# Kernel tuning notes

Measured on AMD Instinct MI355X. Metric: run time of the kernel, lower is better.

## Reference

```python
import jax, jax.numpy as jnp
import numpy as np

B, S, D = 4, 2048, 2048
H = 16
DH = D // H  # 128


def setup_inputs() -> dict:
    key = jax.random.key(0)
    ks = jax.random.split(key, 12)
    s = 1.0 / np.sqrt(D)
    inp = {
        "Q": jax.random.normal(ks[0], (B, S, D), jnp.float32),
        "K": jax.random.normal(ks[1], (B, S, D), jnp.float32),
        "V": jax.random.normal(ks[2], (B, S, D), jnp.float32),
        "mask": jnp.tril(jnp.ones((S, S), jnp.int32))[None, None],  # causal [1,1,S,S]
        "wq": jax.random.uniform(ks[3], (D, D), jnp.float32, -s, s),
        "bq": jax.random.uniform(ks[4], (D,), jnp.float32, -s, s),
        "wk": jax.random.uniform(ks[5], (D, D), jnp.float32, -s, s),
        "bk": jax.random.uniform(ks[6], (D,), jnp.float32, -s, s),
        "wv": jax.random.uniform(ks[7], (D, D), jnp.float32, -s, s),
        "bv": jax.random.uniform(ks[8], (D,), jnp.float32, -s, s),
        "wo": jax.random.uniform(ks[9], (D, D), jnp.float32, -s, s),
        "bo": jax.random.uniform(ks[10], (D,), jnp.float32, -s, s),
    }
    return inp


def _split_heads(x):
    # [B,S,D] -> [B,H,S,DH]
    b, s, _ = x.shape
    return x.reshape(b, s, H, DH).transpose(0, 2, 1, 3)


def reference(Q, K, V, mask, wq, bq, wk, bk, wv, bv, wo, bo):
    q = _split_heads(Q @ wq + bq)
    k = _split_heads(K @ wk + bk)
    v = _split_heads(V @ wv + bv)
    scores = jnp.einsum("bhqd,bhkd->bhqk", q, k) / jnp.sqrt(jnp.float32(DH))
    scores = jnp.where(mask == 0, jnp.float32(-1e9), scores)
    probs = jax.nn.softmax(scores, axis=-1)
    attn = jnp.einsum("bhqk,bhkd->bhqd", probs, v)  # [B,H,S,DH]
    attn = attn.transpose(0, 2, 1, 3).reshape(Q.shape[0], Q.shape[1], D)
    return attn @ wo + bo
```

## Files before the change

kernel.cpp:

```cpp
#include <hip/hip_runtime.h>
#include <hip/hip_bf16.h>

typedef __attribute__((ext_vector_type(8))) short short8;
typedef __attribute__((ext_vector_type(4))) float f32x4;

#define DEVINL __device__ __forceinline__

constexpr int Bc = 4, Sc = 2048, Dc = 2048, Hc = 16, DHc = 128;
constexpr float SCALE = 0.08838834764831845f;

DEVINL short f2bf(float f) {
  unsigned u = __builtin_bit_cast(unsigned, f);
  u = (u + 0x7fffu + ((u >> 16) & 1u)) >> 16;
  return (short)u;
}
DEVINL unsigned pack2(float a, float b) {
  return (unsigned)(unsigned short)f2bf(a) | ((unsigned)(unsigned short)f2bf(b) << 16);
}

DEVINL void gload16(const void* g, void* l) {
  __builtin_amdgcn_global_load_lds(
      (const __attribute__((address_space(1))) void*)g,
      (__attribute__((address_space(3))) void*)l, 16, 0, 0);
}

__global__ __launch_bounds__(256) void transpose_w_kernel(
    const float* __restrict__ w0, const float* __restrict__ w1,
    const float* __restrict__ w2, const float* __restrict__ w3,
    short* __restrict__ wt) {
  __shared__ float tile[32][33];
  const float* w = (blockIdx.z == 0) ? w0 : (blockIdx.z == 1) ? w1
                   : (blockIdx.z == 2) ? w2 : w3;
  short* out = wt + (size_t)blockIdx.z * Dc * Dc;
  int k0 = blockIdx.x * 32, n0 = blockIdx.y * 32;
  int t = threadIdx.x;
#pragma unroll
  for (int p = 0; p < 4; ++p) {
    int idx = p * 256 + t;
    int kr = idx >> 5, nc = idx & 31;
    tile[kr][nc] = w[(size_t)(k0 + kr) * Dc + n0 + nc];
  }
  __syncthreads();
#pragma unroll
  for (int p = 0; p < 4; ++p) {
    int idx = p * 256 + t;
    int nr = idx >> 5, kc = idx & 31;
    out[(size_t)(n0 + nr) * Dc + k0 + kc] = f2bf(tile[kc][nr]);
  }
}

__global__ __launch_bounds__(256) void convert_kernel(
    const float* __restrict__ in, short* __restrict__ out, int n8) {
  int stride = gridDim.x * 256;
  for (int idx = blockIdx.x * 256 + threadIdx.x; idx < n8; idx += stride) {
    const f32x4* p = (const f32x4*)(in + (size_t)idx * 8);
    f32x4 a = p[0], b = p[1];
    short8 r;
    r[0] = f2bf(a[0]); r[1] = f2bf(a[1]); r[2] = f2bf(a[2]); r[3] = f2bf(a[3]);
    r[4] = f2bf(b[0]); r[5] = f2bf(b[1]); r[6] = f2bf(b[2]); r[7] = f2bf(b[3]);
    *(short8*)(out + (size_t)idx * 8) = r;
  }
}

template <int OUT_MODE>
__global__ __launch_bounds__(512, 2) void gemm256_kernel(
    const short* __restrict__ A, const short* __restrict__ Wt,
    const float* __restrict__ bias, void* __restrict__ Cptr) {
  __shared__ __align__(16) short As[2][256 * 64];
  __shared__ __align__(16) short Bs[2][256 * 64];
  const int tid = threadIdx.x, lane = tid & 63, wid = tid >> 6;
  const int wm = wid >> 2, wn = wid & 3;
  const int lr = lane & 15, g = lane >> 4, x7 = lr & 7;

  const int bid = blockIdx.x;
  const int swz = (bid & 7) * 32 + (bid >> 3);
  const int m0 = (swz >> 3) * 256, n0 = (swz & 7) * 256;

  const int srow8 = lane >> 3;
  const int scol = ((lane & 7) ^ srow8) * 8;
  const int arow = m0 + wid * 8 + srow8;
  const int brow = n0 + wid * 8 + srow8;
  const int ldst = wid * 8 * 128;

  auto stageKt = [&](int kt, int slot) {
    const int kof = kt * 64 + scol;
#pragma unroll
    for (int h = 0; h < 2; ++h)
#pragma unroll
      for (int p2 = 0; p2 < 2; ++p2) {
        const int roff = h * 128 + p2 * 64;
        gload16(&A[(size_t)(arow + roff) * Dc + kof],
                (char*)&As[slot][0] + roff * 128 + ldst);
        gload16(&Wt[(size_t)(brow + roff) * Dc + kof],
                (char*)&Bs[slot][0] + roff * 128 + ldst);
      }
  };

  f32x4 acc[8][4] = {};

  stageKt(0, 0);
  asm volatile("s_waitcnt vmcnt(0)" ::: "memory");
  __builtin_amdgcn_s_barrier();

  for (int t = 0; t < 16; ++t) {
#pragma unroll
    for (int half = 0; half < 2; ++half) {
      const short* Ab = &As[half][0];
      const short* Bb = &Bs[half][0];
      short8 afr[4][2], bfr[4][2];
#pragma unroll
      for (int q = 0; q < 4; ++q) {
        if (q == 0) {
#pragma unroll
          for (int i = 0; i < 4; ++i)
#pragma unroll
            for (int kk = 0; kk < 2; ++kk)
              afr[i][kk] = *(const short8*)&Ab[(wm * 128 + i * 16 + lr) * 64 +
                                               (((kk * 4 + g) ^ x7) * 8)];
#pragma unroll
          for (int j = 0; j < 2; ++j)
#pragma unroll
            for (int kk = 0; kk < 2; ++kk)
              bfr[j][kk] = *(const short8*)&Bb[(wn * 64 + j * 16 + lr) * 64 +
                                               (((kk * 4 + g) ^ x7) * 8)];
        } else if (q == 1) {
#pragma unroll
          for (int j = 2; j < 4; ++j)
#pragma unroll
            for (int kk = 0; kk < 2; ++kk)
              bfr[j][kk] = *(const short8*)&Bb[(wn * 64 + j * 16 + lr) * 64 +
                                               (((kk * 4 + g) ^ x7) * 8)];
        } else if (q == 2) {
#pragma unroll
          for (int i = 0; i < 4; ++i)
#pragma unroll
            for (int kk = 0; kk < 2; ++kk)
              afr[i][kk] = *(const short8*)&Ab[(wm * 128 + 64 + i * 16 + lr) * 64 +
                                               (((kk * 4 + g) ^ x7) * 8)];
        }
        if (q == 0) {
          if (half == 0) stageKt(2 * t + 1, 1);
          else if (t < 15) stageKt(2 * t + 2, 0);
        }
        __builtin_amdgcn_s_barrier();
        asm volatile("s_waitcnt lgkmcnt(0)" ::: "memory");
        __builtin_amdgcn_sched_barrier(0);
        __builtin_amdgcn_s_setprio(1);
        const int qr = q >> 1, qc = q & 1;
#pragma unroll
        for (int i = 0; i < 4; ++i)
#pragma unroll
          for (int j = 0; j < 2; ++j)
#pragma unroll
            for (int kk = 0; kk < 2; ++kk)
              acc[qr * 4 + i][qc * 2 + j] = __builtin_amdgcn_mfma_f32_16x16x32_bf16(
                  afr[i][kk], bfr[qc * 2 + j][kk], acc[qr * 4 + i][qc * 2 + j], 0, 0, 0);
        __builtin_amdgcn_s_setprio(0);
        if (q == 3) {
          asm volatile("s_waitcnt vmcnt(0)" ::: "memory");
          __builtin_amdgcn_s_barrier();
        }
      }
    }
  }

  const int rowl = g * 4;
#pragma unroll
  for (int bj = 0; bj < 4; ++bj) {
    const int gcol = n0 + wn * 64 + bj * 16 + lr;
    const float bv = bias[gcol];
#pragma unroll
    for (int ai = 0; ai < 8; ++ai) {
#pragma unroll
      for (int r = 0; r < 4; ++r) {
        int grow = m0 + wm * 128 + ai * 16 + rowl + r;
        float v = acc[ai][bj][r] + bv;
        if (OUT_MODE == 1) {
          ((float*)Cptr)[(size_t)grow * Dc + gcol] = v;
        } else if (OUT_MODE == 0) {
          ((short*)Cptr)[(size_t)grow * Dc + gcol] = f2bf(v);
        } else {
          int b4 = grow >> 11, ss = grow & (Sc - 1);
          int hh = gcol >> 7, dh = gcol & (DHc - 1);
          ((short*)Cptr)[((((size_t)(b4 * Hc + hh) * DHc) + dh) << 11) + ss] = f2bf(v);
        }
      }
    }
  }
}

__global__ __launch_bounds__(512, 2) void attn_kernel(
    const short* __restrict__ qp, const short* __restrict__ kp,
    const short* __restrict__ vt, short* __restrict__ attn) {
  __shared__ __align__(16) short Ks[64 * 128];
  __shared__ __align__(16) short Vs[128 * 64];
  __shared__ __align__(16) short Ps[8][32][72];
  const int tid = threadIdx.x, lane = tid & 63, wid = tid >> 6;
  const int lr = lane & 15, g = lane >> 4, lk = g * 8, rowl = g * 4;
  const int d = blockIdx.x;
  const int xcd = d & 7, s = d >> 3;
  const int grp = s >> 3;
  const int qi = (grp < 4) ? grp : 11 - grp;
  const int bh = xcd * 8 + (s & 7);
  const int b = bh >> 4, h = bh & 15;
  const int qb = qi * 256;
  const size_t headq = ((size_t)b * Sc) * Dc + (size_t)h * DHc;
  const size_t vbase = (((size_t)b * Hc + h) * DHc) << 11;
  const int qw = qb + wid * 32;
  const int x7 = lr & 7;

  short8 qf[2][4];
#pragma unroll
  for (int qs = 0; qs < 2; ++qs)
#pragma unroll
    for (int c = 0; c < 4; ++c)
      qf[qs][c] = *(const short8*)&qp[headq + (size_t)(qw + qs * 16 + lr) * Dc + c * 32 + lk];

  const int krow = wid * 4 + g;
  const int kcol = lr * 8;
  const int vrow = wid * 8 + (lane >> 3);
  const int vcol = (lane & 7) * 8;
  int kdst[2], vdst[2];
#pragma unroll
  for (int p = 0; p < 2; ++p) {
    int kr = p * 32 + krow;
    kdst[p] = kr * 128 + ((lr ^ (kr & 7)) * 8);
    int vr = p * 64 + vrow;
    vdst[p] = vr * 64 + (((lane & 7) ^ (vr & 7)) * 8);
  }

  short8 kreg[2], vreg[2];
  auto issue = [&](int kvb) {
#pragma unroll
    for (int p = 0; p < 2; ++p)
      kreg[p] = *(const short8*)&kp[headq + (size_t)(kvb + p * 32 + krow) * Dc + kcol];
#pragma unroll
    for (int p = 0; p < 2; ++p)
      vreg[p] = *(const short8*)&vt[vbase + (size_t)(p * 64 + vrow) * Sc + kvb + vcol];
  };
  auto commit = [&]() {
#pragma unroll
    for (int p = 0; p < 2; ++p) *(short8*)&Ks[kdst[p]] = kreg[p];
#pragma unroll
    for (int p = 0; p < 2; ++p) *(short8*)&Vs[vdst[p]] = vreg[p];
  };

  issue(0);
  commit();
  __syncthreads();

  f32x4 o[2][8] = {};
  float mrun[2] = {-1e30f, -1e30f}, lrun[2] = {0.f, 0.f};
  const int ntiles = qb / 64 + 4;

  for (int t = 0; t < ntiles; ++t) {
    const bool active = (64 * t <= qw + 31);
    f32x4 sc[2][4];

    if (active) {
      __builtin_amdgcn_s_setprio(1);
#pragma unroll
      for (int nb = 0; nb < 4; ++nb) {
        f32x4 s0 = {}, s1 = {};
#pragma unroll
        for (int c = 0; c < 4; ++c) {
          short8 kf = *(const short8*)&Ks[(nb * 16 + lr) * 128 + (((c * 4 + g) ^ x7) << 3)];
          s0 = __builtin_amdgcn_mfma_f32_16x16x32_bf16(kf, qf[0][c], s0, 0, 0, 0);
          s1 = __builtin_amdgcn_mfma_f32_16x16x32_bf16(kf, qf[1][c], s1, 0, 0, 0);
        }
        sc[0][nb] = s0;
        sc[1][nb] = s1;
      }
      __builtin_amdgcn_s_setprio(0);
    }

    if (t + 1 < ntiles) issue((t + 1) * 64);

    if (active) {
      const bool domask = (64 * t + 63 > qw);
#pragma unroll
      for (int qs = 0; qs < 2; ++qs) {
        const int qg = qw + qs * 16 + lr;
        float mnb[4];
#pragma unroll
        for (int nb = 0; nb < 4; ++nb) {
#pragma unroll
          for (int r = 0; r < 4; ++r) {
            float v = sc[qs][nb][r] * SCALE;
            if (domask) {
              int kv = t * 64 + nb * 16 + rowl + r;
              v = (kv > qg) ? -1e30f : v;
            }
            sc[qs][nb][r] = v;
          }
          mnb[nb] = fmaxf(fmaxf(sc[qs][nb][0], sc[qs][nb][1]),
                          fmaxf(sc[qs][nb][2], sc[qs][nb][3]));
        }
        float mt = fmaxf(fmaxf(mnb[0], mnb[1]), fmaxf(mnb[2], mnb[3]));
        mt = fmaxf(mt, __shfl_xor(mt, 16));
        mt = fmaxf(mt, __shfl_xor(mt, 32));

        float mnew = fmaxf(mrun[qs], mt);
        float alpha = __expf(mrun[qs] - mnew);
        mrun[qs] = mnew;

        float lsnb[4];
#pragma unroll
        for (int nb = 0; nb < 4; ++nb) {
          float p0 = __expf(sc[qs][nb][0] - mnew);
          float p1 = __expf(sc[qs][nb][1] - mnew);
          float p2 = __expf(sc[qs][nb][2] - mnew);
          float p3 = __expf(sc[qs][nb][3] - mnew);
          lsnb[nb] = (p0 + p1) + (p2 + p3);
          uint2 w;
          w.x = pack2(p0, p1);
          w.y = pack2(p2, p3);
          *(uint2*)&Ps[wid][qs * 16 + lr][nb * 16 + rowl] = w;
        }
        float ls = (lsnb[0] + lsnb[1]) + (lsnb[2] + lsnb[3]);
        ls += __shfl_xor(ls, 16);
        ls += __shfl_xor(ls, 32);
        lrun[qs] = lrun[qs] * alpha + ls;

        float al[4];
#pragma unroll
        for (int r = 0; r < 4; ++r) al[r] = __shfl(alpha, (lane & 48) | (rowl + r));
#pragma unroll
        for (int f = 0; f < 8; ++f)
#pragma unroll
          for (int r = 0; r < 4; ++r) o[qs][f][r] *= al[r];
      }

      asm volatile("s_waitcnt lgkmcnt(0)" ::: "memory");
      __builtin_amdgcn_sched_barrier(0);

      __builtin_amdgcn_s_setprio(1);
#pragma unroll
      for (int kc = 0; kc < 2; ++kc) {
        short8 pf0 = *(const short8*)&Ps[wid][lr][kc * 32 + lk];
        short8 pf1 = *(const short8*)&Ps[wid][16 + lr][kc * 32 + lk];
#pragma unroll
        for (int nb = 0; nb < 8; ++nb) {
          short8 vf = *(const short8*)&Vs[(nb * 16 + lr) * 64 + (((kc * 4 + g) ^ x7) << 3)];
          o[0][nb] = __builtin_amdgcn_mfma_f32_16x16x32_bf16(pf0, vf, o[0][nb], 0, 0, 0);
          o[1][nb] = __builtin_amdgcn_mfma_f32_16x16x32_bf16(pf1, vf, o[1][nb], 0, 0, 0);
        }
      }
      __builtin_amdgcn_s_setprio(0);
    }

    __syncthreads();
    if (t + 1 < ntiles) commit();
    __syncthreads();
  }

#pragma unroll
  for (int qs = 0; qs < 2; ++qs) {
    float ld[4];
#pragma unroll
    for (int r = 0; r < 4; ++r) ld[r] = __shfl(lrun[qs], (lane & 48) | (rowl + r));
#pragma unroll
    for (int f = 0; f < 8; ++f)
#pragma unroll
      for (int r = 0; r < 4; ++r) {
        float v = o[qs][f][r] / ld[r];
        attn[headq + (size_t)(qw + qs * 16 + rowl + r) * Dc + f * 16 + lr] = f2bf(v);
      }
  }
}

extern "C" void kernel_launch(void* const* d_in, const int* in_sizes, int n_in,
                              void* d_out, int out_size, void* d_ws, size_t ws_size,
                              hipStream_t stream) {
  const float* Q = (const float*)d_in[0];
  const float* K = (const float*)d_in[1];
  const float* V = (const float*)d_in[2];
  const float* wq = (const float*)d_in[4];
  const float* bq = (const float*)d_in[5];
  const float* wk = (const float*)d_in[6];
  const float* bk = (const float*)d_in[7];
  const float* wv = (const float*)d_in[8];
  const float* bv = (const float*)d_in[9];
  const float* wo = (const float*)d_in[10];
  const float* bo = (const float*)d_in[11];

  char* ws = (char*)d_ws;
  const size_t WSZ = (size_t)Dc * Dc;
  const size_t XSZ = (size_t)Bc * Sc * Dc;
  short* WT = (short*)ws;
  short* QP = (short*)(ws + 4 * WSZ * 2);
  short* KP = (short*)(ws + 4 * WSZ * 2 + XSZ * 2);
  short* VT = (short*)(ws + 4 * WSZ * 2 + 2 * XSZ * 2);
  short* AT = (short*)(ws + 4 * WSZ * 2 + 3 * XSZ * 2);

  transpose_w_kernel<<<dim3(Dc / 32, Dc / 32, 4), 256, 0, stream>>>(wq, wk, wv, wo, WT);

  const int n8 = (int)(XSZ / 8);
  const int ng = (Bc * Sc / 256) * (Dc / 256);

  convert_kernel<<<2048, 256, 0, stream>>>(Q, AT, n8);
  gemm256_kernel<0><<<ng, 512, 0, stream>>>(AT, WT, bq, QP);
  convert_kernel<<<2048, 256, 0, stream>>>(K, AT, n8);
  gemm256_kernel<0><<<ng, 512, 0, stream>>>(AT, WT + WSZ, bk, KP);
  convert_kernel<<<2048, 256, 0, stream>>>(V, AT, n8);
  gemm256_kernel<2><<<ng, 512, 0, stream>>>(AT, WT + 2 * WSZ, bv, VT);

  attn_kernel<<<512, 512, 0, stream>>>(QP, KP, VT, AT);

  gemm256_kernel<1><<<ng, 512, 0, stream>>>(AT, WT + 3 * WSZ, bo, (float*)d_out);
}
```

Baseline: 524.0 us.

## Replace double-buffered GEMM mainloop with 4-slot K=32 ring pipeline

The projection GEMM kernel switches from two 64-wide K stages to a four-slot ring of 32-wide K stages, with three tiles kept in flight. A and B loads for tile kt+3 are issued separately, interleaved with the two MFMA halves, and each iteration waits on a partial vmcnt instead of draining all loads. The aim is to hide global-load latency better and drop the full vmcnt(0) stall. The cost is more barriers per unit of K and a new LDS swizzle that must stay conflict-free.

```diff
diff --git a/kernel.cpp b/kernel.cpp
--- a/kernel.cpp
+++ b/kernel.cpp
@@ -63,105 +63,93 @@
 }
 
 template <int OUT_MODE>
-__global__ __launch_bounds__(512, 2) void gemm256_kernel(
+__global__ __launch_bounds__(512, 2) void gemm_ring_kernel(
     const short* __restrict__ A, const short* __restrict__ Wt,
     const float* __restrict__ bias, void* __restrict__ Cptr) {
-  __shared__ __align__(16) short As[2][256 * 64];
-  __shared__ __align__(16) short Bs[2][256 * 64];
+  __shared__ __align__(16) short As[4][256 * 32];
+  __shared__ __align__(16) short Bs[4][256 * 32];
   const int tid = threadIdx.x, lane = tid & 63, wid = tid >> 6;
   const int wm = wid >> 2, wn = wid & 3;
-  const int lr = lane & 15, g = lane >> 4, x7 = lr & 7;
+  const int lr = lane & 15, g = lane >> 4;
+  const int physg = (g ^ ((lr >> 1) & 3)) * 8;
 
   const int bid = blockIdx.x;
   const int swz = (bid & 7) * 32 + (bid >> 3);
   const int m0 = (swz >> 3) * 256, n0 = (swz & 7) * 256;
 
-  const int srow8 = lane >> 3;
-  const int scol = ((lane & 7) ^ srow8) * 8;
-  const int arow = m0 + wid * 8 + srow8;
-  const int brow = n0 + wid * 8 + srow8;
-  const int ldst = wid * 8 * 128;
-
-  auto stageKt = [&](int kt, int slot) {
-    const int kof = kt * 64 + scol;
-#pragma unroll
-    for (int h = 0; h < 2; ++h)
-#pragma unroll
-      for (int p2 = 0; p2 < 2; ++p2) {
-        const int roff = h * 128 + p2 * 64;
-        gload16(&A[(size_t)(arow + roff) * Dc + kof],
-                (char*)&As[slot][0] + roff * 128 + ldst);
-        gload16(&Wt[(size_t)(brow + roff) * Dc + kof],
-                (char*)&Bs[slot][0] + roff * 128 + ldst);
-      }
+  const int srow = lane >> 2;
+  const int scol = ((lane & 3) ^ ((lane >> 3) & 3)) * 8;
+  const size_t abase = (size_t)(m0 + wid * 32 + srow) * Dc + scol;
+  const size_t bbase = (size_t)(n0 + wid * 32 + srow) * Dc + scol;
+  const int ldof = wid * 32 * 64;
+
+  auto stageA = [&](int kt) {
+    const short* src = &A[abase + kt * 32];
+    char* dst = (char*)&As[kt & 3][0] + ldof;
+    gload16(src, dst);
+    gload16(src + (size_t)16 * Dc, dst + 16 * 64);
   };
+  auto stageB = [&](int kt) {
+    const short* src = &Wt[bbase + kt * 32];
+    char* dst = (char*)&Bs[kt & 3][0] + ldof;
+    gload16(src, dst);
+    gload16(src + (size_t)16 * Dc, dst + 16 * 64);
+  };
 
   f32x4 acc[8][4] = {};
 
-  stageKt(0, 0);
-  asm volatile("s_waitcnt vmcnt(0)" ::: "memory");
+  stageA(0); stageB(0);
+  stageA(1); stageB(1);
+  stageA(2); stageB(2);
+  asm volatile("s_waitcnt vmcnt(8)" ::: "memory");
   __builtin_amdgcn_s_barrier();
 
-  for (int t = 0; t < 16; ++t) {
-#pragma unroll
-    for (int half = 0; half < 2; ++half) {
-      const short* Ab = &As[half][0];
-      const short* Bb = &Bs[half][0];
-      short8 afr[4][2], bfr[4][2];
-#pragma unroll
-      for (int q = 0; q < 4; ++q) {
-        if (q == 0) {
-#pragma unroll
-          for (int i = 0; i < 4; ++i)
-#pragma unroll
-            for (int kk = 0; kk < 2; ++kk)
-              afr[i][kk] = *(const short8*)&Ab[(wm * 128 + i * 16 + lr) * 64 +
-                                               (((kk * 4 + g) ^ x7) * 8)];
-#pragma unroll
-          for (int j = 0; j < 2; ++j)
-#pragma unroll
-            for (int kk = 0; kk < 2; ++kk)
-              bfr[j][kk] = *(const short8*)&Bb[(wn * 64 + j * 16 + lr) * 64 +
-                                               (((kk * 4 + g) ^ x7) * 8)];
-        } else if (q == 1) {
-#pragma unroll
-          for (int j = 2; j < 4; ++j)
-#pragma unroll
-            for (int kk = 0; kk < 2; ++kk)
-              bfr[j][kk] = *(const short8*)&Bb[(wn * 64 + j * 16 + lr) * 64 +
-                                               (((kk * 4 + g) ^ x7) * 8)];
-        } else if (q == 2) {
-#pragma unroll
-          for (int i = 0; i < 4; ++i)
-#pragma unroll
-            for (int kk = 0; kk < 2; ++kk)
-              afr[i][kk] = *(const short8*)&Ab[(wm * 128 + 64 + i * 16 + lr) * 64 +
-                                               (((kk * 4 + g) ^ x7) * 8)];
-        }
-        if (q == 0) {
-          if (half == 0) stageKt(2 * t + 1, 1);
-          else if (t < 15) stageKt(2 * t + 2, 0);
-        }
-        __builtin_amdgcn_s_barrier();
-        asm volatile("s_waitcnt lgkmcnt(0)" ::: "memory");
-        __builtin_amdgcn_sched_barrier(0);
-        __builtin_amdgcn_s_setprio(1);
-        const int qr = q >> 1, qc = q & 1;
-#pragma unroll
-        for (int i = 0; i < 4; ++i)
-#pragma unroll
-          for (int j = 0; j < 2; ++j)
-#pragma unroll
-            for (int kk = 0; kk < 2; ++kk)
-              acc[qr * 4 + i][qc * 2 + j] = __builtin_amdgcn_mfma_f32_16x16x32_bf16(
-                  afr[i][kk], bfr[qc * 2 + j][kk], acc[qr * 4 + i][qc * 2 + j], 0, 0, 0);
-        __builtin_amdgcn_s_setprio(0);
-        if (q == 3) {
-          asm volatile("s_waitcnt vmcnt(0)" ::: "memory");
-          __builtin_amdgcn_s_barrier();
-        }
-      }
+  for (int kt = 0; kt < 64; ++kt) {
+    const short* Ab = &As[kt & 3][0];
+    const short* Bb = &Bs[kt & 3][0];
+    short8 afr[4], bfr[4];
+
+#pragma unroll
+    for (int i = 0; i < 4; ++i)
+      afr[i] = *(const short8*)&Ab[(wm * 128 + i * 16 + lr) * 32 + physg];
+#pragma unroll
+    for (int j = 0; j < 4; ++j)
+      bfr[j] = *(const short8*)&Bb[(wn * 64 + j * 16 + lr) * 32 + physg];
+    if (kt < 61) stageA(kt + 3);
+    __builtin_amdgcn_s_barrier();
+    asm volatile("s_waitcnt lgkmcnt(0)" ::: "memory");
+    __builtin_amdgcn_sched_barrier(0);
+    __builtin_amdgcn_s_setprio(1);
+#pragma unroll
+    for (int i = 0; i < 4; ++i)
+#pragma unroll
+      for (int j = 0; j < 4; ++j)
+        acc[i][j] = __builtin_amdgcn_mfma_f32_16x16x32_bf16(afr[i], bfr[j], acc[i][j], 0, 0, 0);
+    __builtin_amdgcn_s_setprio(0);
+    __builtin_amdgcn_s_barrier();
+
+#pragma unroll
+    for (int i = 0; i < 4; ++i)
+      afr[i] = *(const short8*)&Ab[(wm * 128 + 64 + i * 16 + lr) * 32 + physg];
+    if (kt < 61) stageB(kt + 3);
+    __builtin_amdgcn_s_barrier();
+    asm volatile("s_waitcnt lgkmcnt(0)" ::: "memory");
+    __builtin_amdgcn_sched_barrier(0);
+    __builtin_amdgcn_s_setprio(1);
+#pragma unroll
+    for (int i = 0; i < 4; ++i)
+#pragma unroll
+      for (int j = 0; j < 4; ++j)
+        acc[4 + i][j] = __builtin_amdgcn_mfma_f32_16x16x32_bf16(afr[i], bfr[j], acc[4 + i][j], 0, 0, 0);
+    __builtin_amdgcn_s_setprio(0);
+    if (kt <= 60) {
+      asm volatile("s_waitcnt vmcnt(8)" ::: "memory");
+    } else if (kt == 61) {
+      asm volatile("s_waitcnt vmcnt(4)" ::: "memory");
+    } else if (kt == 62) {
+      asm volatile("s_waitcnt vmcnt(0)" ::: "memory");
     }
+    __builtin_amdgcn_s_barrier();
   }
 
   const int rowl = g * 4;
@@ -399,13 +387,13 @@
   const int ng = (Bc * Sc / 256) * (Dc / 256);
 
   convert_kernel<<<2048, 256, 0, stream>>>(Q, AT, n8);
-  gemm256_kernel<0><<<ng, 512, 0, stream>>>(AT, WT, bq, QP);
+  gemm_ring_kernel<0><<<ng, 512, 0, stream>>>(AT, WT, bq, QP);
   convert_kernel<<<2048, 256, 0, stream>>>(K, AT, n8);
-  gemm256_kernel<0><<<ng, 512, 0, stream>>>(AT, WT + WSZ, bk, KP);
+  gemm_ring_kernel<0><<<ng, 512, 0, stream>>>(AT, WT + WSZ, bk, KP);
   convert_kernel<<<2048, 256, 0, stream>>>(V, AT, n8);
-  gemm256_kernel<2><<<ng, 512, 0, stream>>>(AT, WT + 2 * WSZ, bv, VT);
+  gemm_ring_kernel<2><<<ng, 512, 0, stream>>>(AT, WT + 2 * WSZ, bv, VT);
 
   attn_kernel<<<512, 512, 0, stream>>>(QP, KP, VT, AT);
 
-  gemm256_kernel<1><<<ng, 512, 0, stream>>>(AT, WT + 3 * WSZ, bo, (float*)d_out);
-}
+  gemm_ring_kernel<1><<<ng, 512, 0, stream>>>(AT, WT + 3 * WSZ, bo, (float*)d_out);
+}
```

New measurement: 499.6 us. -4.7%, faster.
